# Kernel optimization log

Measured on AMD Instinct MI355X. Metric: run time of the kernel, lower is better.

The kernel has to match this reference:

```python
import jax, jax.numpy as jnp
import numpy as np

N = 50000       # nodes
F_IN = 256
F_OUT = 64
H = 4           # heads
DEG = 16        # avg degree (random edges per node)
NEG_SLOPE = 0.2


def setup_inputs() -> dict:
    key = jax.random.key(0)
    k_h, k_e, k_w, k_fc = jax.random.split(key, 4)
    h = jax.random.normal(k_h, (N, F_IN), dtype=jnp.float32)
    # random edges + explicit self-loops so every node has >= 1 out-edge
    e_rand = jax.random.randint(k_e, (2, N * DEG), 0, N, dtype=jnp.int64)
    loops = jnp.tile(jnp.arange(N, dtype=jnp.int64)[None, :], (2, 1))
    edge_index = jnp.concatenate([e_rand, loops], axis=1)  # [2, 850000]
    # Glorot-uniform-like scales
    s_w = np.sqrt(6.0 / (F_IN + F_OUT)).astype(np.float32)
    s_a = np.sqrt(6.0 / (2 * F_OUT + 1)).astype(np.float32)
    w = jax.random.uniform(k_w, (H, F_IN, F_OUT), jnp.float32, -s_w, s_w)
    fc = jax.random.uniform(k_fc, (H, 2 * F_OUT, 1), jnp.float32, -s_a, s_a)
    bias = jnp.zeros((F_OUT,), jnp.float32)
    return {"h": h, "edge_index": edge_index, "w": w, "fc": fc, "bias": bias}


def reference(h, edge_index, w, fc, bias):
    # GAT forward, vectorized over edges (dropout is identity at inference).
    n = h.shape[0]
    f_out = w.shape[2]
    src, dst = edge_index[0], edge_index[1]           # [E]
    h_prime = jnp.einsum('nf,hfo->hno', h, w)          # [H, N, F]
    a = fc[..., 0]                                     # [H, 2F]
    a_src, a_dst = a[:, :f_out], a[:, f_out:]          # [H, F] each
    s_src = jnp.einsum('hnf,hf->hn', h_prime, a_src)   # [H, N] score of center node
    s_dst = jnp.einsum('hnf,hf->hn', h_prime, a_dst)   # [H, N] score of neighbor
    e = jax.nn.leaky_relu(s_src[:, src] + s_dst[:, dst], NEG_SLOPE)  # [H, E]
    e = e.T                                            # [E, H]
    # segment softmax over edges grouped by source node
    seg_max = jax.ops.segment_max(e, src, num_segments=n)   # [N, H]
    ex = jnp.exp(e - seg_max[src])                           # [E, H]
    denom = jax.ops.segment_sum(ex, src, num_segments=n)    # [N, H]
    alpha = ex / denom[src]                                  # [E, H]
    # scatter-aggregate: out_i = sum_{j in N(i)} alpha_ij * Wh_j
    msgs = alpha[:, :, None] * jnp.transpose(h_prime[:, dst, :], (1, 0, 2))  # [E, H, F]
    out = jax.ops.segment_sum(msgs, src, num_segments=n)    # [N, H, F]
    return out.mean(axis=1) + bias                           # [N, F]
```

## Files before the change

### kernel.cpp

```cpp
#include <hip/hip_runtime.h>
#include <cfloat>

#define FIN 256
#define FOUT 64
#define NH 4
#define NEG_SLOPE 0.2f
#define SLOTS 64
#define BCAP 3072
#define P1T 4096

typedef __bf16 bf16x8 __attribute__((ext_vector_type(8)));
typedef float f32x4 __attribute__((ext_vector_type(4)));

__device__ __forceinline__ ushort f2bf(float f) {
    return (ushort)((__float_as_uint(f) + 0x8000u) >> 16);
}
__device__ __forceinline__ float bf2f(ushort u) {
    return __uint_as_float(((unsigned)u) << 16);
}
__device__ __forceinline__ float lrelu(float x) {
    return (x >= 0.f) ? x : NEG_SLOPE * x;
}

__global__ __launch_bounds__(256) void k0_wconv(const float* __restrict__ w,
                                                ushort* __restrict__ wt,
                                                int* __restrict__ gcur, int gn)
{
    if ((int)blockIdx.x < 256) {
        const int g = blockIdx.x * 256 + threadIdx.x;
        const int hh  = g >> 14;
        const int rem = g & 16383;
        const int c   = rem >> 8;
        const int k   = rem & 255;
        wt[g] = f2bf(w[(((hh << 8) | k) << 6) | c]);
    } else {
        const int g = ((int)blockIdx.x - 256) * 256 + threadIdx.x;
        if (g < gn) gcur[g] = 0;
    }
}

__global__ __launch_bounds__(256) void k1a(
    const int* __restrict__ ei, int E, int nbuck,
    int* __restrict__ gcur, unsigned* __restrict__ barea)
{
    __shared__ int lcnt[512];
    __shared__ int lscan[512];
    __shared__ int lbase[512];
    __shared__ unsigned ledges[P1T];
    const int tid = threadIdx.x;

    for (int b = tid; b < 512; b += 256) lcnt[b] = 0;
    __syncthreads();

    const int e0 = (int)blockIdx.x * P1T;
    const int cnt_total = min(P1T, E - e0);
    int s[16], d[16];
#pragma unroll
    for (int i = 0; i < 16; ++i) {
        const int e = e0 + i * 256 + tid;
        if (e < E) {
            s[i] = ei[e];
            d[i] = ei[E + e];
            atomicAdd(&lcnt[s[i] >> 7], 1);
        } else {
            s[i] = -1; d[i] = 0;
        }
    }
    __syncthreads();

    if (tid < 64) {
        int vals[8], sum = 0;
#pragma unroll
        for (int k = 0; k < 8; ++k) { vals[k] = lcnt[tid * 8 + k]; sum += vals[k]; }
        int x = sum;
#pragma unroll
        for (int dd = 1; dd < 64; dd <<= 1) {
            const int t = __shfl_up(x, dd);
            if (tid >= dd) x += t;
        }
        int run = x - sum;
#pragma unroll
        for (int k = 0; k < 8; ++k) { lscan[tid * 8 + k] = run; run += vals[k]; }
    }
    __syncthreads();

    for (int b = tid; b < nbuck; b += 256) {
        const int c = lcnt[b];
        lbase[b] = c ? atomicAdd(&gcur[b * 16], c) : 0;
    }
    __syncthreads();
    for (int b = tid; b < 512; b += 256) lcnt[b] = 0;
    __syncthreads();

#pragma unroll
    for (int i = 0; i < 16; ++i) {
        if (s[i] >= 0) {
            const int b = s[i] >> 7;
            const int r = atomicAdd(&lcnt[b], 1);
            ledges[lscan[b] + r] =
                ((unsigned)b << 23) | ((unsigned)(s[i] & 127) << 16) |
                (unsigned)d[i];
        }
    }
    __syncthreads();

    for (int j = tid; j < cnt_total; j += 256) {
        const unsigned p = ledges[j];
        const int b = (int)(p >> 23);
        const int pos = lbase[b] + (j - lscan[b]);
        if (pos < BCAP)
            barea[(size_t)b * BCAP + pos] = p & 0x007FFFFFu;
    }
}

#define ASTRIDE 280
#define OSTRIDE 260
__global__ __launch_bounds__(256) void k_gemm(
    const float* __restrict__ h, const ushort* __restrict__ wt,
    const float* __restrict__ fc, ushort* __restrict__ hp,
    float* __restrict__ s_src, float* __restrict__ s_dst, int N)
{
    __shared__ ushort lds[64 * ASTRIDE];
    const int tid = threadIdx.x;
    const int n0 = (int)blockIdx.x * 64;

#pragma unroll
    for (int half = 0; half < 2; ++half) {
        float4 va[8];
#pragma unroll
        for (int i = 0; i < 8; ++i) {
            const int idx = half * 2048 + i * 256 + tid;
            const int row  = idx >> 6;
            const int quad = idx & 63;
            const int n = n0 + row;
            va[i] = (n < N) ? ((const float4*)(h + (size_t)n * FIN))[quad]
                            : make_float4(0.f, 0.f, 0.f, 0.f);
        }
#pragma unroll
        for (int i = 0; i < 8; ++i) {
            const int idx = half * 2048 + i * 256 + tid;
            const int row  = idx >> 6;
            const int quad = idx & 63;
            ushort4 bv;
            bv.x = f2bf(va[i].x); bv.y = f2bf(va[i].y);
            bv.z = f2bf(va[i].z); bv.w = f2bf(va[i].w);
            *(ushort4*)&lds[row * ASTRIDE + quad * 4] = bv;
        }
    }
    __syncthreads();

    const int head = tid >> 6;
    const int lane = tid & 63;
    const int lrow = lane & 15;
    const int lq   = lane >> 4;

    const ushort* wth = wt + head * (64 * 256);

    f32x4 acc[4][4];
#pragma unroll
    for (int mt = 0; mt < 4; ++mt)
#pragma unroll
        for (int nt = 0; nt < 4; ++nt)
            acc[mt][nt] = (f32x4){0.f, 0.f, 0.f, 0.f};

    bf16x8 bcur[4], bnxt[4];
#pragma unroll
    for (int nt = 0; nt < 4; ++nt)
        bcur[nt] = *(const bf16x8*)&wth[(nt * 16 + lrow) * 256 + lq * 8];

#pragma unroll
    for (int kt = 0; kt < 8; ++kt) {
        const int kof = kt * 32 + lq * 8;
        if (kt < 7) {
            const int kof2 = kof + 32;
#pragma unroll
            for (int nt = 0; nt < 4; ++nt)
                bnxt[nt] = *(const bf16x8*)&wth[(nt * 16 + lrow) * 256 + kof2];
        }
        bf16x8 af[4];
#pragma unroll
        for (int mt = 0; mt < 4; ++mt)
            af[mt] = *(const bf16x8*)&lds[(mt * 16 + lrow) * ASTRIDE + kof];
#pragma unroll
        for (int nt = 0; nt < 4; ++nt)
#pragma unroll
            for (int mt = 0; mt < 4; ++mt)
                acc[mt][nt] = __builtin_amdgcn_mfma_f32_16x16x32_bf16(
                    af[mt], bcur[nt], acc[mt][nt], 0, 0, 0);
#pragma unroll
        for (int nt = 0; nt < 4; ++nt) bcur[nt] = bnxt[nt];
    }

    float as_[4], ad_[4];
#pragma unroll
    for (int nt = 0; nt < 4; ++nt) {
        as_[nt] = fc[head * 2 * FOUT + nt * 16 + lrow];
        ad_[nt] = fc[head * 2 * FOUT + FOUT + nt * 16 + lrow];
    }
#pragma unroll
    for (int mt = 0; mt < 4; ++mt) {
        const int rbase = n0 + mt * 16 + lq * 4;
#pragma unroll
        for (int r = 0; r < 4; ++r) {
            const int n = rbase + r;
            float ps = 0.f, pd = 0.f;
#pragma unroll
            for (int nt = 0; nt < 4; ++nt) {
                const float v = acc[mt][nt][r];
                ps = fmaf(v, as_[nt], ps);
                pd = fmaf(v, ad_[nt], pd);
            }
            ps += __shfl_xor(ps, 1); pd += __shfl_xor(pd, 1);
            ps += __shfl_xor(ps, 2); pd += __shfl_xor(pd, 2);
            ps += __shfl_xor(ps, 4); pd += __shfl_xor(pd, 4);
            ps += __shfl_xor(ps, 8); pd += __shfl_xor(pd, 8);
            if (lrow == 0 && n < N) {
                s_src[(size_t)n * NH + head] = ps;
                s_dst[(size_t)n * NH + head] = pd;
            }
        }
    }

    __syncthreads();
#pragma unroll
    for (int mt = 0; mt < 4; ++mt)
#pragma unroll
        for (int r = 0; r < 4; ++r)
#pragma unroll
            for (int nt = 0; nt < 4; ++nt)
                lds[(mt * 16 + lq * 4 + r) * OSTRIDE +
                    (nt * 16 + lrow) * 4 + head] = f2bf(acc[mt][nt][r]);
    __syncthreads();
    for (int idx = tid; idx < 64 * 64; idx += 256) {
        const int row = idx >> 6;
        const int c   = idx & 63;
        const int n = n0 + row;
        if (n < N)
            *(ushort4*)&hp[(size_t)n * 256 + c * 4] =
                *(const ushort4*)&lds[row * OSTRIDE + c * 4];
    }
}

__global__ __launch_bounds__(256) void k2(
    const int* __restrict__ gcur, const unsigned* __restrict__ barea,
    ushort* __restrict__ col, int* __restrict__ cursor)
{
    __shared__ ushort colT[128 * SLOTS];
    __shared__ int cnt[128];
    const int tid = threadIdx.x;
    const int b = blockIdx.x;
    for (int i = tid; i < 128; i += 256) cnt[i] = 0;
    __syncthreads();
    int c = gcur[b * 16];
    if (c > BCAP) c = BCAP;
    for (int j = tid; j < c; j += 256) {
        const unsigned p = barea[(size_t)b * BCAP + j];
        const int sl = (int)((p >> 16) & 127);
        const int r = atomicAdd(&cnt[sl], 1);
        if (r < SLOTS) colT[sl * SLOTS + r] = (ushort)(p & 0xFFFFu);
    }
    __syncthreads();
    const size_t gbase = (size_t)b * 128 * SLOTS;
    for (int idx = tid; idx < 128 * SLOTS / 4; idx += 256)
        *(ushort4*)&col[gbase + (size_t)idx * 4] =
            *(const ushort4*)&colT[idx * 4];
    for (int i = tid; i < 128; i += 256)
        cursor[b * 128 + i] = cnt[i];
}

__global__ __launch_bounds__(256) void k_agg(
    const int* __restrict__ cursor, const ushort* __restrict__ col,
    const ushort* __restrict__ hp,
    const float* __restrict__ s_src, const float* __restrict__ s_dst,
    const float* __restrict__ bias, float* __restrict__ out, int N, int base)
{
    const int wid  = threadIdx.x >> 6;
    const int lane = threadIdx.x & 63;
    const int n    = base + blockIdx.x * 4 + wid;
    if (n >= N) return;

    const size_t start = (size_t)n * SLOTS;
    const int deg = min(cursor[n], SLOTS);
    const float4 ssn = ((const float4*)s_src)[n];
    const float4* sd4 = (const float4*)s_dst;

    float4 acc = make_float4(0.f, 0.f, 0.f, 0.f);

    int dreg = 0;
    float4 x = make_float4(-FLT_MAX, -FLT_MAX, -FLT_MAX, -FLT_MAX);
    if (lane < deg) {
        dreg = col[start + lane];
        const float4 sd = sd4[dreg];
        x.x = lrelu(ssn.x + sd.x);
        x.y = lrelu(ssn.y + sd.y);
        x.z = lrelu(ssn.z + sd.z);
        x.w = lrelu(ssn.w + sd.w);
    }
    float4 m = x;
#pragma unroll
    for (int d = 32; d; d >>= 1) {
        m.x = fmaxf(m.x, __shfl_xor(m.x, d));
        m.y = fmaxf(m.y, __shfl_xor(m.y, d));
        m.z = fmaxf(m.z, __shfl_xor(m.z, d));
        m.w = fmaxf(m.w, __shfl_xor(m.w, d));
    }
    float4 e = make_float4(0.f, 0.f, 0.f, 0.f);
    if (lane < deg) {
        e.x = __expf(x.x - m.x);
        e.y = __expf(x.y - m.y);
        e.z = __expf(x.z - m.z);
        e.w = __expf(x.w - m.w);
    }
    float4 s = e;
#pragma unroll
    for (int d = 32; d; d >>= 1) {
        s.x += __shfl_xor(s.x, d);
        s.y += __shfl_xor(s.y, d);
        s.z += __shfl_xor(s.z, d);
        s.w += __shfl_xor(s.w, d);
    }
    float4 alpha;
    alpha.x = e.x / s.x;
    alpha.y = e.y / s.y;
    alpha.z = e.z / s.z;
    alpha.w = e.w / s.w;

    const int nblk = (deg + 3) >> 2;
    for (int b = 0; b < nblk; ++b) {
        int dd[4]; float4 av[4]; ushort4 v[4];
#pragma unroll
        for (int u = 0; u < 4; ++u) {
            const int j = b * 4 + u;
            dd[u]   = __shfl(dreg, j);
            av[u].x = __shfl(alpha.x, j);
            av[u].y = __shfl(alpha.y, j);
            av[u].z = __shfl(alpha.z, j);
            av[u].w = __shfl(alpha.w, j);
        }
#pragma unroll
        for (int u = 0; u < 4; ++u)
            v[u] = *(const ushort4*)&hp[((size_t)dd[u] * FOUT + lane) * NH];
#pragma unroll
        for (int u = 0; u < 4; ++u) {
            acc.x = fmaf(av[u].x, bf2f(v[u].x), acc.x);
            acc.y = fmaf(av[u].y, bf2f(v[u].y), acc.y);
            acc.z = fmaf(av[u].z, bf2f(v[u].z), acc.z);
            acc.w = fmaf(av[u].w, bf2f(v[u].w), acc.w);
        }
    }

    out[(size_t)n * FOUT + lane] =
        (acc.x + acc.y + acc.z + acc.w) * 0.25f + bias[lane];
}

extern "C" void kernel_launch(void* const* d_in, const int* in_sizes, int n_in,
                              void* d_out, int out_size, void* d_ws, size_t ws_size,
                              hipStream_t stream)
{
    const float* h    = (const float*)d_in[0];
    const int*   ei   = (const int*)d_in[1];
    const float* w    = (const float*)d_in[2];
    const float* fc   = (const float*)d_in[3];
    const float* bias = (const float*)d_in[4];
    float* out = (float*)d_out;

    const int N = in_sizes[0] / FIN;
    const int E = in_sizes[1] / 2;
    const int nbuck = (N + 127) >> 7;

    char* ws = (char*)d_ws;
    auto take = [&](size_t bytes) {
        char* p = ws;
        ws += (bytes + 255) & ~(size_t)255;
        return p;
    };
    ushort*   wt      = (ushort*)take((size_t)NH * FIN * FOUT * sizeof(ushort));
    ushort*   h_prime = (ushort*)take((size_t)NH * N * FOUT * sizeof(ushort));
    float*    s_src   = (float*)take((size_t)NH * N * sizeof(float));
    float*    s_dst   = (float*)take((size_t)NH * N * sizeof(float));
    int*      cursor  = (int*)take((size_t)nbuck * 128 * sizeof(int));
    ushort*   col     = (ushort*)take((size_t)nbuck * 128 * SLOTS * sizeof(ushort));
    int*      gcur    = (int*)take((size_t)nbuck * 16 * sizeof(int));
    unsigned* barea   = (unsigned*)take((size_t)nbuck * BCAP * sizeof(unsigned));

    const int gn = nbuck * 16;
    k0_wconv<<<256 + (gn + 255) / 256, 256, 0, stream>>>(w, wt, gcur, gn);

    const int p1B = (E + P1T - 1) / P1T;
    k1a<<<p1B, 256, 0, stream>>>(ei, E, nbuck, gcur, barea);

    k_gemm<<<(N + 63) / 64, 256, 0, stream>>>(h, wt, fc, h_prime,
                                              s_src, s_dst, N);

    k2<<<nbuck, 256, 0, stream>>>(gcur, barea, col, cursor);

    const int total_blocks = (N + 3) / 4;
    const int hb = total_blocks / 2;
    k_agg<<<hb, 256, 0, stream>>>(cursor, col, h_prime, s_src, s_dst,
                                  bias, out, N, 0);
    k_agg<<<total_blocks - hb, 256, 0, stream>>>(cursor, col, h_prime,
                                                 s_src, s_dst, bias, out, N, hb * 4);
}
```

Measured before the change: 151.0 us.

## Split GEMM block across 8 waves and merge aggregation into one launch

The GEMM kernel now runs 512 threads per block. Each head is handled by two waves, each covering half of the 64 rows, which raises the number of waves per block and gives fewer accumulators per wave. The register double-buffering of the B fragments is removed. The two split aggregation launches are merged into a single launch, saving one kernel launch. The tradeoff is less latency hiding from the dropped prefetch, and each W fragment is now loaded by two waves instead of one.

```diff
diff --git a/kernel.cpp b/kernel.cpp
--- a/kernel.cpp
+++ b/kernel.cpp
@@ -115,7 +115,7 @@
 
 #define ASTRIDE 280
 #define OSTRIDE 260
-__global__ __launch_bounds__(256) void k_gemm(
+__global__ __launch_bounds__(512) void k_gemm(
     const float* __restrict__ h, const ushort* __restrict__ wt,
     const float* __restrict__ fc, ushort* __restrict__ hp,
     float* __restrict__ s_src, float* __restrict__ s_dst, int N)
@@ -124,12 +124,11 @@
     const int tid = threadIdx.x;
     const int n0 = (int)blockIdx.x * 64;
 
-#pragma unroll
-    for (int half = 0; half < 2; ++half) {
+    {
         float4 va[8];
 #pragma unroll
         for (int i = 0; i < 8; ++i) {
-            const int idx = half * 2048 + i * 256 + tid;
+            const int idx = i * 512 + tid;
             const int row  = idx >> 6;
             const int quad = idx & 63;
             const int n = n0 + row;
@@ -138,7 +137,7 @@
         }
 #pragma unroll
         for (int i = 0; i < 8; ++i) {
-            const int idx = half * 2048 + i * 256 + tid;
+            const int idx = i * 512 + tid;
             const int row  = idx >> 6;
             const int quad = idx & 63;
             ushort4 bv;
@@ -149,46 +148,40 @@
     }
     __syncthreads();
 
-    const int head = tid >> 6;
-    const int lane = tid & 63;
-    const int lrow = lane & 15;
-    const int lq   = lane >> 4;
+    const int wid   = tid >> 6;
+    const int head  = wid & 3;
+    const int mhalf = wid >> 2;
+    const int lane  = tid & 63;
+    const int lrow  = lane & 15;
+    const int lq    = lane >> 4;
 
     const ushort* wth = wt + head * (64 * 256);
 
-    f32x4 acc[4][4];
-#pragma unroll
-    for (int mt = 0; mt < 4; ++mt)
+    f32x4 acc[2][4];
+#pragma unroll
+    for (int mt = 0; mt < 2; ++mt)
 #pragma unroll
         for (int nt = 0; nt < 4; ++nt)
             acc[mt][nt] = (f32x4){0.f, 0.f, 0.f, 0.f};
 
-    bf16x8 bcur[4], bnxt[4];
-#pragma unroll
-    for (int nt = 0; nt < 4; ++nt)
-        bcur[nt] = *(const bf16x8*)&wth[(nt * 16 + lrow) * 256 + lq * 8];
-
 #pragma unroll
     for (int kt = 0; kt < 8; ++kt) {
         const int kof = kt * 32 + lq * 8;
-        if (kt < 7) {
-            const int kof2 = kof + 32;
-#pragma unroll
-            for (int nt = 0; nt < 4; ++nt)
-                bnxt[nt] = *(const bf16x8*)&wth[(nt * 16 + lrow) * 256 + kof2];
-        }
-        bf16x8 af[4];
-#pragma unroll
-        for (int mt = 0; mt < 4; ++mt)
-            af[mt] = *(const bf16x8*)&lds[(mt * 16 + lrow) * ASTRIDE + kof];
+        bf16x8 bfr[4];
 #pragma unroll
         for (int nt = 0; nt < 4; ++nt)
-#pragma unroll
-            for (int mt = 0; mt < 4; ++mt)
+            bfr[nt] = *(const bf16x8*)&wth[(nt * 16 + lrow) * 256 + kof];
+        bf16x8 af[2];
+#pragma unroll
+        for (int mt = 0; mt < 2; ++mt)
+            af[mt] = *(const bf16x8*)
+                &lds[(mhalf * 32 + mt * 16 + lrow) * ASTRIDE + kof];
+#pragma unroll
+        for (int nt = 0; nt < 4; ++nt)
+#pragma unroll
+            for (int mt = 0; mt < 2; ++mt)
                 acc[mt][nt] = __builtin_amdgcn_mfma_f32_16x16x32_bf16(
-                    af[mt], bcur[nt], acc[mt][nt], 0, 0, 0);
-#pragma unroll
-        for (int nt = 0; nt < 4; ++nt) bcur[nt] = bnxt[nt];
+                    af[mt], bfr[nt], acc[mt][nt], 0, 0, 0);
     }
 
     float as_[4], ad_[4];
@@ -198,8 +191,8 @@
         ad_[nt] = fc[head * 2 * FOUT + FOUT + nt * 16 + lrow];
     }
 #pragma unroll
-    for (int mt = 0; mt < 4; ++mt) {
-        const int rbase = n0 + mt * 16 + lq * 4;
+    for (int mt = 0; mt < 2; ++mt) {
+        const int rbase = n0 + mhalf * 32 + mt * 16 + lq * 4;
 #pragma unroll
         for (int r = 0; r < 4; ++r) {
             const int n = rbase + r;
@@ -223,15 +216,15 @@
 
     __syncthreads();
 #pragma unroll
-    for (int mt = 0; mt < 4; ++mt)
+    for (int mt = 0; mt < 2; ++mt)
 #pragma unroll
         for (int r = 0; r < 4; ++r)
 #pragma unroll
             for (int nt = 0; nt < 4; ++nt)
-                lds[(mt * 16 + lq * 4 + r) * OSTRIDE +
+                lds[(mhalf * 32 + mt * 16 + lq * 4 + r) * OSTRIDE +
                     (nt * 16 + lrow) * 4 + head] = f2bf(acc[mt][nt][r]);
     __syncthreads();
-    for (int idx = tid; idx < 64 * 64; idx += 256) {
+    for (int idx = tid; idx < 64 * 64; idx += 512) {
         const int row = idx >> 6;
         const int c   = idx & 63;
         const int n = n0 + row;
@@ -272,11 +265,11 @@
     const int* __restrict__ cursor, const ushort* __restrict__ col,
     const ushort* __restrict__ hp,
     const float* __restrict__ s_src, const float* __restrict__ s_dst,
-    const float* __restrict__ bias, float* __restrict__ out, int N, int base)
+    const float* __restrict__ bias, float* __restrict__ out, int N)
 {
     const int wid  = threadIdx.x >> 6;
     const int lane = threadIdx.x & 63;
-    const int n    = base + blockIdx.x * 4 + wid;
+    const int n    = blockIdx.x * 4 + wid;
     if (n >= N) return;
 
     const size_t start = (size_t)n * SLOTS;
@@ -389,15 +382,11 @@
     const int p1B = (E + P1T - 1) / P1T;
     k1a<<<p1B, 256, 0, stream>>>(ei, E, nbuck, gcur, barea);
 
-    k_gemm<<<(N + 63) / 64, 256, 0, stream>>>(h, wt, fc, h_prime,
+    k_gemm<<<(N + 63) / 64, 512, 0, stream>>>(h, wt, fc, h_prime,
                                               s_src, s_dst, N);
 
     k2<<<nbuck, 256, 0, stream>>>(gcur, barea, col, cursor);
 
-    const int total_blocks = (N + 3) / 4;
-    const int hb = total_blocks / 2;
-    k_agg<<<hb, 256, 0, stream>>>(cursor, col, h_prime, s_src, s_dst,
-                                  bias, out, N, 0);
-    k_agg<<<total_blocks - hb, 256, 0, stream>>>(cursor, col, h_prime,
-                                                 s_src, s_dst, bias, out, N, hb * 4);
-}
+    k_agg<<<(N + 3) / 4, 256, 0, stream>>>(cursor, col, h_prime,
+                                           s_src, s_dst, bias, out, N);
+}
```

New measurement: 151.6 us. About the same (+0.4%).
